# Optimization experiments

Measured on AMD Instinct MI355X. Metric: run time of the kernel, lower is better.

## Reference

```python
import jax, jax.numpy as jnp
import numpy as np

N_WIRES = 16
N_LAYERS = 4
BATCH = 256
DIM = 2 ** N_WIRES


def _rot_u(theta):
    # theta: (3,) = (rx, ry, rz) angles. Combined single-qubit unitary
    # U = RZ(rz) @ RY(ry) @ RX(rx), matching the gate application order
    # RX -> RY -> RZ in the circuit.
    a, b, c = theta[0] * 0.5, theta[1] * 0.5, theta[2] * 0.5
    cx = jnp.cos(a).astype(jnp.complex64)
    sx = jnp.sin(a).astype(jnp.complex64)
    cy = jnp.cos(b).astype(jnp.complex64)
    sy = jnp.sin(b).astype(jnp.complex64)
    RX = jnp.stack([jnp.stack([cx, -1j * sx]), jnp.stack([-1j * sx, cx])])
    RY = jnp.stack([jnp.stack([cy, -sy]), jnp.stack([sy, cy])])
    ez = jnp.exp(-1j * c.astype(jnp.complex64))
    RZ = jnp.stack([jnp.stack([ez, 0 * ez]), jnp.stack([0 * ez, jnp.conj(ez)])])
    return RZ @ (RY @ RX)


def _apply_1q(psi, U, q):
    # psi: [B] + [2]*n ; apply 2x2 unitary U on qubit axis q
    psi = jnp.moveaxis(psi, 1 + q, -1)
    psi = psi @ U.T  # new[i] = sum_j U[i,j] psi[j]
    return jnp.moveaxis(psi, -1, 1 + q)


def _apply_cnot(psi, c, t):
    # control qubit c, target qubit t
    psi = jnp.moveaxis(psi, (1 + c, 1 + t), (-2, -1))  # [..., 2(c), 2(t)]
    psi = jnp.stack([psi[..., 0, :], psi[..., 1, ::-1]], axis=-2)
    return jnp.moveaxis(psi, (-2, -1), (1 + c, 1 + t))


def _forward(state_batch, params, w_head, b_head):
    B = state_batch.shape[0]
    psi = state_batch.astype(jnp.complex64).reshape((B,) + (2,) * N_WIRES)
    # Precompute all fused RZ*RY*RX unitaries: [L, n, 2, 2]
    Us = jax.vmap(jax.vmap(_rot_u))(params)
    for layer in range(N_LAYERS):
        for q in range(N_WIRES):
            psi = _apply_1q(psi, Us[layer, q], q)
        for q in range(N_WIRES - 1):
            psi = _apply_cnot(psi, q, q + 1)
    psi = psi.reshape(B, DIM)
    probs = psi.real ** 2 + psi.imag ** 2  # [B, DIM], float32
    # PauliZ expectation per wire; wire 0 is the most significant bit
    idx = jnp.arange(DIM)[:, None]
    bits = (idx >> (N_WIRES - 1 - jnp.arange(N_WIRES))) & 1  # [DIM, n]
    signs = (1 - 2 * bits).astype(jnp.float32)
    features = probs @ signs  # [B, n]
    out = features @ w_head.T + b_head  # [B, 1]
    return out[:, 0]


def setup_inputs() -> dict:
    key = jax.random.key(0)
    k1, k2, k3, k4 = jax.random.split(key, 4)
    state = jax.random.normal(k1, (BATCH, DIM), jnp.float32)
    state = state / jnp.linalg.norm(state, axis=-1, keepdims=True)
    params = jax.random.normal(k2, (N_LAYERS, N_WIRES, 3), jnp.float32)
    w_head = jax.random.normal(k3, (1, N_WIRES), jnp.float32) / np.float32(np.sqrt(N_WIRES))
    b_head = jax.random.normal(k4, (1,), jnp.float32) * 0.01
    return {"state_batch": state, "params": params, "w_head": w_head, "b_head": b_head}


def reference(state_batch, params, w_head, b_head):
    return _forward(state_batch, params, w_head, b_head)
```

## Files before the change

kernel.cpp:

```cpp
#include <hip/hip_runtime.h>

typedef float v2f __attribute__((ext_vector_type(2)));

#define NW 16
#define NBATCH 256
#define QDIM 65536

__device__ __forceinline__ int swz(int l) { return l ^ ((l >> 5) & 31); }

__device__ __forceinline__ void rot2(v2f& x, v2f& y, v2f aa, v2f an, v2f bb, v2f bn) {
  v2f xs = __builtin_shufflevector(x, x, 1, 0);
  v2f ys = __builtin_shufflevector(y, y, 1, 0);
  v2f n0 = aa * x + an * xs + bb * y + bn * ys;
  v2f n1 = aa * y - an * ys + bn * xs - bb * x;
  x = n0;
  y = n1;
}

#define ROT(T, G)                                                              \
  do {                                                                         \
    const float4 u = Utab[G];                                                  \
    const v2f aa = {u.x, u.x}, an = {-u.y, u.y};                               \
    const v2f bb = {u.z, u.z}, bn = {-u.w, u.w};                               \
    _Pragma("unroll") for (int v = 0; v < 32; ++v) if (!((v >> (T)) & 1))      \
        rot2(s[v], s[v | (1 << (T))], aa, an, bb, bn);                         \
  } while (0)

#define CNOTW(C, T)                                                            \
  do {                                                                         \
    _Pragma("unroll") for (int v = 0; v < 32; ++v)                             \
        if (((v >> (C)) & 1) && !((v >> (T)) & 1)) {                           \
      v2f tmp = s[v];                                                          \
      s[v] = s[v | (1 << (T))];                                                \
      s[v | (1 << (T))] = tmp;                                                 \
    }                                                                          \
  } while (0)

#define MAP_W1(t, v) (((v) << 8) | (t))
#define MAP_W2(t, v) ((((t) >> 4) << 9) | ((v) << 4) | ((t) & 15))
#define MAP_W3(t, v) (((t) << 5) | (v))
#define MAP_M1(t, v) ((((t) >> 1) << 6) | ((v) << 1) | ((t) & 1))
#define MAP_M2(t, v) ((((t) >> 2) << 7) | ((v) << 2) | ((t) & 3))

#define REMAP(MW, MR)                                                          \
  do {                                                                         \
    _Pragma("unroll") for (int r = 0; r < 32; ++r)                             \
        lds2[swz(MW(tid, r))] = s[r];                                          \
    __syncthreads();                                                           \
    _Pragma("unroll") for (int v = 0; v < 32; ++v)                             \
        s[v] = lds2[swz(MR(tid, v))];                                          \
    __syncthreads();                                                           \
  } while (0)

__global__ void k_setup(const float* __restrict__ params, float4* __restrict__ Utab) {
  int g = threadIdx.x;
  if (g < 64) {
    float a = params[g * 3 + 0] * 0.5f;
    float b = params[g * 3 + 1] * 0.5f;
    float c = params[g * 3 + 2] * 0.5f;
    float sa, ca, sb, cb, sc, cc;
    sincosf(a, &sa, &ca);
    sincosf(b, &sb, &cb);
    sincosf(c, &sc, &cc);
    float X = cb * ca, Y = sb * sa;
    float Xp = -sb * ca, Yp = -cb * sa;
    Utab[g] = make_float4(cc * X + sc * Y, cc * Y - sc * X,
                          cc * Xp + sc * Yp, cc * Yp - sc * Xp);
  }
}

__global__ __launch_bounds__(256, 2) void k_passA(const float* __restrict__ in,
                                                  const float4* __restrict__ Utab,
                                                  v2f* __restrict__ st) {
  __shared__ v2f lds2[8192];
  const int tid = threadIdx.x;
  const int g = blockIdx.x >> 8;
  const int b = blockIdx.x & 255;
  const float* base = in + (size_t)b * QDIM;

  v2f s[32];
#pragma unroll
  for (int v = 0; v < 32; ++v) {
    float re = base[(MAP_W1(tid, v) << 3) | g];
    s[v] = v2f{re, 0.0f};
  }

  for (int l = 0; l < 4; ++l) {
    ROT(4, l * 16 + 0); ROT(3, l * 16 + 1); ROT(2, l * 16 + 2);
    ROT(1, l * 16 + 3); ROT(0, l * 16 + 4);
    CNOTW(4, 3); CNOTW(3, 2); CNOTW(2, 1); CNOTW(1, 0);
    REMAP(MAP_W1, MAP_W2);
    ROT(3, l * 16 + 5); ROT(2, l * 16 + 6); ROT(1, l * 16 + 7); ROT(0, l * 16 + 8);
    CNOTW(4, 3); CNOTW(3, 2); CNOTW(2, 1); CNOTW(1, 0);
    REMAP(MAP_W2, MAP_W3);
    ROT(3, l * 16 + 9);
    if (l <= 2) ROT(2, l * 16 + 10);
    if (l <= 1) ROT(1, l * 16 + 11);
    if (l == 0) ROT(0, l * 16 + 12);
    CNOTW(4, 3);
    if (l <= 2) CNOTW(3, 2);
    if (l <= 1) CNOTW(2, 1);
    if (l == 0) CNOTW(1, 0);
    if (l < 3) REMAP(MAP_W3, MAP_W1);
  }

#pragma unroll
  for (int r = 0; r < 32; ++r) lds2[swz(MAP_W3(tid, r))] = s[r];
  __syncthreads();
  v2f* outp = st + (size_t)(b * 8 + g) * 8192;
#pragma unroll
  for (int k = 0; k < 32; ++k) outp[k * 256 + tid] = lds2[swz(k * 256 + tid)];
}

__global__ __launch_bounds__(256, 2) void k_passB(const v2f* __restrict__ st,
                                                  const float4* __restrict__ Utab,
                                                  float* __restrict__ partials) {
  __shared__ v2f lds2[8192];
  const int tid = threadIdx.x;
  const int b = blockIdx.x >> 3;
  const int h = blockIdx.x & 7;
  const v2f* base = st + (size_t)b * 8 * 8192;

#pragma unroll
  for (int k = 0; k < 32; ++k) {
    int o = k * 256 + tid;
    v2f val = base[((o >> 10) << 13) + (h << 10) + (o & 1023)];
    lds2[swz(((o & 1023) << 3) | (o >> 10))] = val;
  }
  __syncthreads();
  v2f s[32];
#pragma unroll
  for (int v = 0; v < 32; ++v) s[v] = lds2[swz(MAP_W3(tid, v))];
  __syncthreads();

  ROT(2, 13); ROT(1, 14); ROT(0, 15);
  CNOTW(3, 2); CNOTW(2, 1); CNOTW(1, 0);
  ROT(3, 16 + 12); ROT(2, 16 + 13); ROT(1, 16 + 14); ROT(0, 16 + 15);
  CNOTW(4, 3); CNOTW(3, 2); CNOTW(2, 1); CNOTW(1, 0);
  ROT(4, 32 + 11); ROT(3, 32 + 12); ROT(2, 32 + 13);
  ROT(1, 32 + 14); ROT(0, 32 + 15);
  REMAP(MAP_W3, MAP_M1);
  CNOTW(4, 3); CNOTW(3, 2); CNOTW(2, 1); CNOTW(1, 0);
  ROT(4, 48 + 10); ROT(3, 48 + 11); ROT(2, 48 + 12); ROT(1, 48 + 13);
  REMAP(MAP_M1, MAP_M2);
  CNOTW(4, 3); CNOTW(3, 2); CNOTW(2, 1); CNOTW(1, 0);
  REMAP(MAP_M2, MAP_W3);
  CNOTW(1, 0);
  ROT(1, 48 + 14); ROT(0, 48 + 15);
  CNOTW(2, 1);
  CNOTW(1, 0);

  float P = 0.f, f11 = 0.f, f12 = 0.f, f13 = 0.f, f14 = 0.f, f15 = 0.f;
#pragma unroll
  for (int r = 0; r < 32; ++r) {
    float p = s[r][0] * s[r][0] + s[r][1] * s[r][1];
    P += p;
    f11 += ((r >> 4) & 1) ? -p : p;
    f12 += ((r >> 3) & 1) ? -p : p;
    f13 += ((r >> 2) & 1) ? -p : p;
    f14 += ((r >> 1) & 1) ? -p : p;
    f15 += ((r >> 0) & 1) ? -p : p;
  }
  float vals[14];
  vals[0] = P;
#pragma unroll
  for (int q = 3; q <= 10; ++q)
    vals[q - 2] = ((tid >> (10 - q)) & 1) ? -P : P;
  vals[9] = f11; vals[10] = f12; vals[11] = f13; vals[12] = f14; vals[13] = f15;

  float* red = (float*)lds2;
#pragma unroll
  for (int q = 0; q < 14; ++q) red[q * 256 + tid] = vals[q];
  __syncthreads();
  for (int off = 128; off > 0; off >>= 1) {
    if (tid < off) {
#pragma unroll
      for (int q = 0; q < 14; ++q) red[q * 256 + tid] += red[q * 256 + tid + off];
    }
    __syncthreads();
  }
  if (tid == 0) {
    float Pt = red[0];
    float* pt = partials + (size_t)blockIdx.x * 16;
    pt[0] = (h & 4) ? -Pt : Pt;
    pt[1] = (h & 2) ? -Pt : Pt;
    pt[2] = (h & 1) ? -Pt : Pt;
#pragma unroll
    for (int q = 3; q <= 15; ++q) pt[q] = red[(q - 2) * 256];
  }
}

__global__ void k_head(const float* __restrict__ partials, const float* __restrict__ w,
                       const float* __restrict__ bh, float* __restrict__ out) {
  int b = threadIdx.x;
  float acc = bh[0];
  for (int q = 0; q < 16; ++q) {
    float F = 0.f;
    for (int hh = 0; hh < 8; ++hh) F += partials[(size_t)(b * 8 + hh) * 16 + q];
    acc += w[q] * F;
  }
  out[b] = acc;
}

extern "C" void kernel_launch(void* const* d_in, const int* in_sizes, int n_in,
                              void* d_out, int out_size, void* d_ws, size_t ws_size,
                              hipStream_t stream) {
  const float* state  = (const float*)d_in[0];
  const float* params = (const float*)d_in[1];
  const float* w_head = (const float*)d_in[2];
  const float* b_head = (const float*)d_in[3];
  float* out = (float*)d_out;

  char* ws = (char*)d_ws;
  v2f* st = (v2f*)ws;
  float4* Utab = (float4*)(ws + (size_t)134217728);
  float* partials = (float*)(ws + (size_t)134217728 + 1024);

  k_setup<<<1, 64, 0, stream>>>(params, Utab);
  k_passA<<<dim3(2048), dim3(256), 0, stream>>>(state, Utab, st);
  k_passB<<<dim3(2048), dim3(256), 0, stream>>>(st, Utab, partials);
  k_head<<<1, 256, 0, stream>>>(partials, w_head, b_head, out);
}
```

Baseline: 226.0 us.

## Use 512-thread blocks with 16 amplitudes per thread and restructure gate schedule

Doubles the threads per block and halves the amplitudes held per thread, so the gate sequence in both passes is reorganised around 4-bit register windows with more LDS remap steps. This lowers register pressure and raises occupancy, at the cost of extra LDS round-trips and barriers. It also widens global stores and loads to float4, remaps the block index so neighbouring blocks share batch locality, and swaps the LDS tree reduction for wavefront shuffle reductions.

```diff
diff --git a/kernel.cpp b/kernel.cpp
--- a/kernel.cpp
+++ b/kernel.cpp
@@ -2,9 +2,8 @@
 
 typedef float v2f __attribute__((ext_vector_type(2)));
 
-#define NW 16
-#define NBATCH 256
-#define QDIM 65536
+#define NT 512
+#define NR 16
 
 __device__ __forceinline__ int swz(int l) { return l ^ ((l >> 5) & 31); }
 
@@ -22,13 +21,13 @@
     const float4 u = Utab[G];                                                  \
     const v2f aa = {u.x, u.x}, an = {-u.y, u.y};                               \
     const v2f bb = {u.z, u.z}, bn = {-u.w, u.w};                               \
-    _Pragma("unroll") for (int v = 0; v < 32; ++v) if (!((v >> (T)) & 1))      \
+    _Pragma("unroll") for (int v = 0; v < NR; ++v) if (!((v >> (T)) & 1))      \
         rot2(s[v], s[v | (1 << (T))], aa, an, bb, bn);                         \
   } while (0)
 
 #define CNOTW(C, T)                                                            \
   do {                                                                         \
-    _Pragma("unroll") for (int v = 0; v < 32; ++v)                             \
+    _Pragma("unroll") for (int v = 0; v < NR; ++v)                             \
         if (((v >> (C)) & 1) && !((v >> (T)) & 1)) {                           \
       v2f tmp = s[v];                                                          \
       s[v] = s[v | (1 << (T))];                                                \
@@ -36,18 +35,19 @@
     }                                                                          \
   } while (0)
 
-#define MAP_W1(t, v) (((v) << 8) | (t))
-#define MAP_W2(t, v) ((((t) >> 4) << 9) | ((v) << 4) | ((t) & 15))
-#define MAP_W3(t, v) (((t) << 5) | (v))
-#define MAP_M1(t, v) ((((t) >> 1) << 6) | ((v) << 1) | ((t) & 1))
-#define MAP_M2(t, v) ((((t) >> 2) << 7) | ((v) << 2) | ((t) & 3))
+#define MAP_A1(t, v) (((v) << 9) | (t))
+#define MAP_A2(t, v) ((((t) >> 6) << 10) | ((v) << 6) | ((t) & 63))
+#define MAP_A3(t, v) ((((t) >> 3) << 7) | ((v) << 3) | ((t) & 7))
+#define MAP_A4(t, v) (((t) << 4) | (v))
+#define MAP_B2(t, v) ((((t) >> 2) << 6) | ((v) << 2) | ((t) & 3))
+#define MAP_B3(t, v) ((((t) >> 1) << 5) | ((v) << 1) | ((t) & 1))
 
 #define REMAP(MW, MR)                                                          \
   do {                                                                         \
-    _Pragma("unroll") for (int r = 0; r < 32; ++r)                             \
+    _Pragma("unroll") for (int r = 0; r < NR; ++r)                             \
         lds2[swz(MW(tid, r))] = s[r];                                          \
     __syncthreads();                                                           \
-    _Pragma("unroll") for (int v = 0; v < 32; ++v)                             \
+    _Pragma("unroll") for (int v = 0; v < NR; ++v)                             \
         s[v] = lds2[swz(MR(tid, v))];                                          \
     __syncthreads();                                                           \
   } while (0)
@@ -69,124 +69,149 @@
   }
 }
 
-__global__ __launch_bounds__(256, 2) void k_passA(const float* __restrict__ in,
-                                                  const float4* __restrict__ Utab,
-                                                  v2f* __restrict__ st) {
+__global__ __launch_bounds__(NT, 4) void k_passA(const float* __restrict__ in,
+                                                 const float4* __restrict__ Utab,
+                                                 v2f* __restrict__ st) {
   __shared__ v2f lds2[8192];
   const int tid = threadIdx.x;
-  const int g = blockIdx.x >> 8;
-  const int b = blockIdx.x & 255;
-  const float* base = in + (size_t)b * QDIM;
-
-  v2f s[32];
-#pragma unroll
-  for (int v = 0; v < 32; ++v) {
-    float re = base[(MAP_W1(tid, v) << 3) | g];
+  const int g = (blockIdx.x >> 3) & 7;
+  const int b = ((blockIdx.x >> 6) << 3) | (blockIdx.x & 7);
+  const float* base = in + (size_t)b * 65536;
+
+  v2f s[NR];
+#pragma unroll
+  for (int v = 0; v < NR; ++v) {
+    float re = base[(v << 12) + (tid << 3) + g];
     s[v] = v2f{re, 0.0f};
   }
 
+#pragma unroll
   for (int l = 0; l < 4; ++l) {
-    ROT(4, l * 16 + 0); ROT(3, l * 16 + 1); ROT(2, l * 16 + 2);
-    ROT(1, l * 16 + 3); ROT(0, l * 16 + 4);
-    CNOTW(4, 3); CNOTW(3, 2); CNOTW(2, 1); CNOTW(1, 0);
-    REMAP(MAP_W1, MAP_W2);
-    ROT(3, l * 16 + 5); ROT(2, l * 16 + 6); ROT(1, l * 16 + 7); ROT(0, l * 16 + 8);
-    CNOTW(4, 3); CNOTW(3, 2); CNOTW(2, 1); CNOTW(1, 0);
-    REMAP(MAP_W2, MAP_W3);
-    ROT(3, l * 16 + 9);
-    if (l <= 2) ROT(2, l * 16 + 10);
-    if (l <= 1) ROT(1, l * 16 + 11);
-    if (l == 0) ROT(0, l * 16 + 12);
-    CNOTW(4, 3);
-    if (l <= 2) CNOTW(3, 2);
-    if (l <= 1) CNOTW(2, 1);
-    if (l == 0) CNOTW(1, 0);
-    if (l < 3) REMAP(MAP_W3, MAP_W1);
-  }
-
-#pragma unroll
-  for (int r = 0; r < 32; ++r) lds2[swz(MAP_W3(tid, r))] = s[r];
-  __syncthreads();
-  v2f* outp = st + (size_t)(b * 8 + g) * 8192;
-#pragma unroll
-  for (int k = 0; k < 32; ++k) outp[k * 256 + tid] = lds2[swz(k * 256 + tid)];
-}
-
-__global__ __launch_bounds__(256, 2) void k_passB(const v2f* __restrict__ st,
-                                                  const float4* __restrict__ Utab,
-                                                  float* __restrict__ partials) {
+    ROT(3, l * 16 + 0); ROT(2, l * 16 + 1); ROT(1, l * 16 + 2); ROT(0, l * 16 + 3);
+    CNOTW(3, 2); CNOTW(2, 1); CNOTW(1, 0);
+    REMAP(MAP_A1, MAP_A2);
+    ROT(2, l * 16 + 4); ROT(1, l * 16 + 5); ROT(0, l * 16 + 6);
+    CNOTW(3, 2); CNOTW(2, 1); CNOTW(1, 0);
+    REMAP(MAP_A2, MAP_A3);
+    ROT(2, l * 16 + 7); ROT(1, l * 16 + 8); ROT(0, l * 16 + 9);
+    CNOTW(3, 2); CNOTW(2, 1); CNOTW(1, 0);
+    if (l < 3) {
+      REMAP(MAP_A3, MAP_A4);
+      ROT(2, l * 16 + 10);
+      if (l <= 1) ROT(1, l * 16 + 11);
+      if (l == 0) ROT(0, l * 16 + 12);
+      CNOTW(3, 2);
+      if (l <= 1) CNOTW(2, 1);
+      if (l == 0) CNOTW(1, 0);
+      REMAP(MAP_A4, MAP_A1);
+    }
+  }
+
+#pragma unroll
+  for (int r = 0; r < NR; ++r) lds2[swz(MAP_A3(tid, r))] = s[r];
+  __syncthreads();
+  float4* outp = (float4*)(st + (size_t)(b * 8 + g) * 8192);
+#pragma unroll
+  for (int k = 0; k < 8; ++k) {
+    int o = (k << 10) + (tid << 1);
+    v2f a0 = lds2[swz(o)], a1 = lds2[swz(o + 1)];
+    outp[(k << 9) + tid] = make_float4(a0[0], a0[1], a1[0], a1[1]);
+  }
+}
+
+__global__ __launch_bounds__(NT, 4) void k_passB(const v2f* __restrict__ st,
+                                                 const float4* __restrict__ Utab,
+                                                 float* __restrict__ partials) {
   __shared__ v2f lds2[8192];
   const int tid = threadIdx.x;
   const int b = blockIdx.x >> 3;
   const int h = blockIdx.x & 7;
-  const v2f* base = st + (size_t)b * 8 * 8192;
-
-#pragma unroll
-  for (int k = 0; k < 32; ++k) {
-    int o = k * 256 + tid;
-    v2f val = base[((o >> 10) << 13) + (h << 10) + (o & 1023)];
-    lds2[swz(((o & 1023) << 3) | (o >> 10))] = val;
-  }
-  __syncthreads();
-  v2f s[32];
-#pragma unroll
-  for (int v = 0; v < 32; ++v) s[v] = lds2[swz(MAP_W3(tid, v))];
+  const float4* base4 = (const float4*)(st + (size_t)b * 65536);
+
+#pragma unroll
+  for (int k = 0; k < 8; ++k) {
+    float4 val = base4[(k << 12) + (h << 9) + tid];
+    int i = tid << 1;
+    lds2[swz(((i) << 3) | k)] = v2f{val.x, val.y};
+    lds2[swz(((i + 1) << 3) | k)] = v2f{val.z, val.w};
+  }
+  __syncthreads();
+  v2f s[NR];
+#pragma unroll
+  for (int v = 0; v < NR; ++v) s[v] = lds2[swz(MAP_A4(tid, v))];
   __syncthreads();
 
   ROT(2, 13); ROT(1, 14); ROT(0, 15);
   CNOTW(3, 2); CNOTW(2, 1); CNOTW(1, 0);
-  ROT(3, 16 + 12); ROT(2, 16 + 13); ROT(1, 16 + 14); ROT(0, 16 + 15);
-  CNOTW(4, 3); CNOTW(3, 2); CNOTW(2, 1); CNOTW(1, 0);
-  ROT(4, 32 + 11); ROT(3, 32 + 12); ROT(2, 32 + 13);
-  ROT(1, 32 + 14); ROT(0, 32 + 15);
-  REMAP(MAP_W3, MAP_M1);
-  CNOTW(4, 3); CNOTW(3, 2); CNOTW(2, 1); CNOTW(1, 0);
-  ROT(4, 48 + 10); ROT(3, 48 + 11); ROT(2, 48 + 12); ROT(1, 48 + 13);
-  REMAP(MAP_M1, MAP_M2);
-  CNOTW(4, 3); CNOTW(3, 2); CNOTW(2, 1); CNOTW(1, 0);
-  REMAP(MAP_M2, MAP_W3);
-  CNOTW(1, 0);
-  ROT(1, 48 + 14); ROT(0, 48 + 15);
+  ROT(3, 28); ROT(2, 29); ROT(1, 30); ROT(0, 31);
+  REMAP(MAP_A4, MAP_A3);
+  CNOTW(1, 0);
+  ROT(1, 43);
   CNOTW(2, 1);
-  CNOTW(1, 0);
-
-  float P = 0.f, f11 = 0.f, f12 = 0.f, f13 = 0.f, f14 = 0.f, f15 = 0.f;
-#pragma unroll
-  for (int r = 0; r < 32; ++r) {
-    float p = s[r][0] * s[r][0] + s[r][1] * s[r][1];
+  ROT(2, 58);
+  CNOTW(3, 2);
+  REMAP(MAP_A3, MAP_B2);
+  CNOTW(1, 0);
+  ROT(1, 44);
+  CNOTW(2, 1);
+  ROT(2, 59);
+  CNOTW(3, 2);
+  REMAP(MAP_B2, MAP_B3);
+  CNOTW(1, 0);
+  ROT(1, 45);
+  CNOTW(2, 1);
+  ROT(2, 60);
+  CNOTW(3, 2);
+  REMAP(MAP_B3, MAP_A4);
+  CNOTW(1, 0);
+  ROT(1, 46); ROT(0, 47);
+  CNOTW(2, 1); CNOTW(1, 0);
+  ROT(2, 61); ROT(1, 62); ROT(0, 63);
+  CNOTW(3, 2); CNOTW(2, 1); CNOTW(1, 0);
+
+  float P = 0.f, f12 = 0.f, f13 = 0.f, f14 = 0.f, f15 = 0.f;
+#pragma unroll
+  for (int v = 0; v < NR; ++v) {
+    float p = s[v][0] * s[v][0] + s[v][1] * s[v][1];
     P += p;
-    f11 += ((r >> 4) & 1) ? -p : p;
-    f12 += ((r >> 3) & 1) ? -p : p;
-    f13 += ((r >> 2) & 1) ? -p : p;
-    f14 += ((r >> 1) & 1) ? -p : p;
-    f15 += ((r >> 0) & 1) ? -p : p;
+    f12 += ((v >> 3) & 1) ? -p : p;
+    f13 += ((v >> 2) & 1) ? -p : p;
+    f14 += ((v >> 1) & 1) ? -p : p;
+    f15 += ((v >> 0) & 1) ? -p : p;
   }
   float vals[14];
   vals[0] = P;
 #pragma unroll
-  for (int q = 3; q <= 10; ++q)
-    vals[q - 2] = ((tid >> (10 - q)) & 1) ? -P : P;
-  vals[9] = f11; vals[10] = f12; vals[11] = f13; vals[12] = f14; vals[13] = f15;
-
+  for (int q = 3; q <= 11; ++q)
+    vals[q - 2] = ((tid >> (11 - q)) & 1) ? -P : P;
+  vals[10] = f12; vals[11] = f13; vals[12] = f14; vals[13] = f15;
+
+  const int lane = tid & 63, w = tid >> 6;
+#pragma unroll
+  for (int q = 0; q < 14; ++q) {
+    float x = vals[q];
+#pragma unroll
+    for (int m = 1; m < 64; m <<= 1) x += __shfl_xor(x, m, 64);
+    vals[q] = x;
+  }
   float* red = (float*)lds2;
-#pragma unroll
-  for (int q = 0; q < 14; ++q) red[q * 256 + tid] = vals[q];
-  __syncthreads();
-  for (int off = 128; off > 0; off >>= 1) {
-    if (tid < off) {
-#pragma unroll
-      for (int q = 0; q < 14; ++q) red[q * 256 + tid] += red[q * 256 + tid + off];
+  if (lane == 0) {
+#pragma unroll
+    for (int q = 0; q < 14; ++q) red[q * 8 + w] = vals[q];
+  }
+  __syncthreads();
+  if (tid < 14) {
+    float F = 0.f;
+#pragma unroll
+    for (int ww = 0; ww < 8; ++ww) F += red[tid * 8 + ww];
+    float* pt = partials + (size_t)blockIdx.x * 16;
+    if (tid == 0) {
+      pt[0] = (h & 4) ? -F : F;
+      pt[1] = (h & 2) ? -F : F;
+      pt[2] = (h & 1) ? -F : F;
+    } else {
+      pt[tid + 2] = F;
     }
-    __syncthreads();
-  }
-  if (tid == 0) {
-    float Pt = red[0];
-    float* pt = partials + (size_t)blockIdx.x * 16;
-    pt[0] = (h & 4) ? -Pt : Pt;
-    pt[1] = (h & 2) ? -Pt : Pt;
-    pt[2] = (h & 1) ? -Pt : Pt;
-#pragma unroll
-    for (int q = 3; q <= 15; ++q) pt[q] = red[(q - 2) * 256];
   }
 }
 
@@ -217,7 +242,7 @@
   float* partials = (float*)(ws + (size_t)134217728 + 1024);
 
   k_setup<<<1, 64, 0, stream>>>(params, Utab);
-  k_passA<<<dim3(2048), dim3(256), 0, stream>>>(state, Utab, st);
-  k_passB<<<dim3(2048), dim3(256), 0, stream>>>(st, Utab, partials);
+  k_passA<<<dim3(2048), dim3(NT), 0, stream>>>(state, Utab, st);
+  k_passB<<<dim3(2048), dim3(NT), 0, stream>>>(st, Utab, partials);
   k_head<<<1, 256, 0, stream>>>(partials, w_head, b_head, out);
 }
```

After: 215.1 us. -4.8%, faster.
